# Optimization experiments

Hardware: AMD Instinct MI355X
Metric: run time of the kernel (lower is better)

Reference implementation:

```python
import jax, jax.numpy as jnp
import numpy as np
from jax import lax

NH = 8        # num_heads
NWIN = 7      # n_win
TOPK = 4


def setup_inputs() -> dict:
    key = jax.random.key(0)
    ks = jax.random.split(key, 7)
    B, C, H, W = 16, 256, 56, 56
    x = jax.random.normal(ks[0], (B, C, H, W), dtype=jnp.float32)
    s = 1.0 / np.sqrt(C)
    qkv_w = jax.random.normal(ks[1], (3 * C, C), dtype=jnp.float32) * s   # 1x1 conv
    qkv_b = jnp.zeros((3 * C,), dtype=jnp.float32)
    lepe_w = jax.random.normal(ks[2], (C, 1, 5, 5), dtype=jnp.float32) * 0.2  # depthwise 5x5
    lepe_b = jnp.zeros((C,), dtype=jnp.float32)
    out_w = jax.random.normal(ks[3], (C, C), dtype=jnp.float32) * s       # 1x1 conv
    out_b = jnp.zeros((C,), dtype=jnp.float32)
    return {"x": x, "qkv_w": qkv_w, "qkv_b": qkv_b, "lepe_w": lepe_w,
            "lepe_b": lepe_b, "out_w": out_w, "out_b": out_b}


def reference(x, qkv_w, qkv_b, lepe_w, lepe_b, out_w, out_b):
    B, C, H, W = x.shape
    rs0, rs1 = max(1, H // NWIN), max(1, W // NWIN)   # region size (H,W assumed divisible)
    rh, rw = H // rs0, W // rs1
    nreg, reg = rh * rw, rs0 * rs1
    hd = C // NH
    scale = C ** (-0.5)

    # qkv projection (1x1 conv == channel matmul)
    qkv = jnp.einsum('bchw,oc->bohw', x, qkv_w) + qkv_b[None, :, None, None]
    q, k, v = jnp.split(qkv, 3, axis=1)

    # region-level pooling (avg_pool over exact region blocks)
    def pool(t):
        return t.reshape(B, C, rh, rs0, rw, rs1).mean(axis=(3, 5))  # (B,C,rh,rw)
    q_r = pool(q).reshape(B, C, nreg).transpose(0, 2, 1)   # (B, nreg, C)
    k_r = pool(k).reshape(B, C, nreg)                      # (B, C, nreg)
    a_r = q_r @ k_r                                        # (B, nreg, nreg)
    _, idx = lax.top_k(a_r, TOPK)                          # (B, nreg, topk)

    # grid -> sequence: (B,C,H,W) -> (B,NH,nreg,reg,hd)
    def g2s(t):
        t = t.reshape(B, NH, hd, rh, rs0, rw, rs1)
        t = t.transpose(0, 1, 3, 5, 4, 6, 2)  # b,m,h,w,p,q,d
        return t.reshape(B, NH, nreg, reg, hd)

    qs, ks_, vs = g2s(q), g2s(k), g2s(v)

    # gather top-k kv regions per query region
    idx_h = jnp.broadcast_to(idx[:, None], (B, NH, nreg, TOPK))
    gidx = idx_h.reshape(B, NH, nreg * TOPK)[..., None, None]   # (B,NH,nreg*topk,1,1)
    kg = jnp.take_along_axis(ks_, gidx, axis=2).reshape(B, NH, nreg, TOPK * reg, hd)
    vg = jnp.take_along_axis(vs, gidx, axis=2).reshape(B, NH, nreg, TOPK * reg, hd)

    attn = jax.nn.softmax(jnp.einsum('bhnrd,bhnkd->bhnrk', qs * scale, kg), axis=-1)
    out = jnp.einsum('bhnrk,bhnkd->bhnrd', attn, vg)  # (B,NH,nreg,reg,hd)

    # sequence -> grid
    out = out.reshape(B, NH, rh, rw, rs0, rs1, hd)
    out = out.transpose(0, 1, 6, 2, 4, 3, 5).reshape(B, C, H, W)

    # LePE: depthwise 5x5 conv on v
    lepe = lax.conv_general_dilated(v, lepe_w, (1, 1), 'SAME',
                                    feature_group_count=C,
                                    dimension_numbers=('NCHW', 'OIHW', 'NCHW'))
    lepe = lepe + lepe_b[None, :, None, None]

    out = out + lepe
    out = jnp.einsum('bchw,oc->bohw', out, out_w) + out_b[None, :, None, None]
    return out
```

## Files before the change

### kernel.cpp

```cpp
#include <hip/hip_runtime.h>

typedef __attribute__((ext_vector_type(8))) short short8;
typedef __attribute__((ext_vector_type(4))) float f32x4;
typedef unsigned int uint;

constexpr int Bn    = 16;
constexpr int Cn    = 256;
constexpr int Hn    = 56;
constexpr int Wn    = 56;
constexpr int HWn   = Hn * Wn;
constexpr int NPn   = 3200;
constexpr int NHn   = 8;
constexpr int RWn   = 7;
constexpr int NREGn = 49;
constexpr int TOPKn = 4;
constexpr float QKSf = 0.0625f * 1.44269504088896f;

__device__ __forceinline__ float b2f(ushort u) { return __builtin_bit_cast(float, (uint)u << 16); }
__device__ __forceinline__ float b2fl(uint u) { return __builtin_bit_cast(float, u << 16); }
__device__ __forceinline__ float b2fh(uint u) { return __builtin_bit_cast(float, u & 0xffff0000u); }
__device__ __forceinline__ uint cvtpk(float lo, float hi) {
    uint r;
    asm("v_cvt_pk_bf16_f32 %0, %1, %2" : "=v"(r) : "v"(lo), "v"(hi));
    return r;
}

typedef __attribute__((address_space(3))) uint lds_u32_t;
typedef __attribute__((address_space(1))) const uint glb_u32_t;
__device__ __forceinline__ void gl_lds16(const ushort* g, ushort* l) {
    __builtin_amdgcn_global_load_lds((glb_u32_t*)g, (lds_u32_t*)l, 16, 0, 0);
}

__global__ __launch_bounds__(256)
void convert_w(const float* __restrict__ qw, const float* __restrict__ ow,
               ushort* __restrict__ wq, ushort* __restrict__ wo)
{
    const int e = (blockIdx.x * 256 + threadIdx.x) * 4;
    if (e < 196608) {
        const float4 v = *(const float4*)(qw + e);
        uint2 w; w.x = cvtpk(v.x, v.y); w.y = cvtpk(v.z, v.w);
        *(uint2*)(wq + e) = w;
    } else {
        const int e2 = e - 196608;
        const float4 v = *(const float4*)(ow + e2);
        uint2 w; w.x = cvtpk(v.x, v.y); w.y = cvtpk(v.z, v.w);
        *(uint2*)(wo + e2) = w;
    }
}

__global__ __launch_bounds__(256)
void convert_x(const float* __restrict__ x, ushort* __restrict__ xt,
               float* __restrict__ part)
{
    __shared__ float tile[64][65];
    const int p0 = blockIdx.x * 64, c0 = blockIdx.y * 64, b = blockIdx.z;
    const int tid = threadIdx.x;
    #pragma unroll
    for (int it = 0; it < 4; ++it) {
        const int slot = it * 256 + tid;
        const int c = slot >> 4, p4 = (slot & 15) << 2;
        const float4 v = *(const float4*)(x + ((size_t)b * Cn + c0 + c) * HWn + p0 + p4);
        tile[c][p4 + 0] = v.x; tile[c][p4 + 1] = v.y;
        tile[c][p4 + 2] = v.z; tile[c][p4 + 3] = v.w;
    }
    __syncthreads();
    #pragma unroll
    for (int it = 0; it < 4; ++it) {
        const int slot = it * 256 + tid;
        const int p = slot >> 4, c4 = (slot & 15) << 2;
        uint2 w;
        w.x = cvtpk(tile[c4 + 0][p], tile[c4 + 1][p]);
        w.y = cvtpk(tile[c4 + 2][p], tile[c4 + 3][p]);
        *(uint2*)(xt + ((size_t)b * NPn + p0 + p) * Cn + c0 + c4) = w;
    }
    {
        const int c = tid >> 2, q = tid & 3;
        float sA = 0.f, sB = 0.f;
        #pragma unroll
        for (int p = 0; p < 8; ++p) sA += tile[c][q * 16 + p];
        #pragma unroll
        for (int p = 0; p < 8; ++p) sB += tile[c][q * 16 + 8 + p];
        float* pp = part + ((((size_t)b * 4 + blockIdx.y) * 49 + blockIdx.x) * 64 + c) * 8 + q * 2;
        *(float2*)pp = make_float2(sA, sB);
    }
}

__global__ __launch_bounds__(256)
void reduce_pool(const float* __restrict__ part, float* __restrict__ xr)
{
    const int gid = blockIdx.x * 256 + threadIdx.x;
    const int r = gid % NREGn;
    const int t = gid / NREGn;
    const int c = t % Cn, b = t / Cn;
    const int ry = r / 7, rx = r % 7;
    const float* pb = part + ((((size_t)b * 4 + (c >> 6)) * 49 + 7 * ry) * 64 + (c & 63)) * 8;
    float s = 0.f;
    #pragma unroll
    for (int j = 0; j < 7; ++j) {
        const int s0 = (rx - j + 7) % 7;
        s += pb[j * 512 + s0];
        if (s0 == 0) s += pb[j * 512 + 7];
    }
    xr[gid] = s * (1.0f / 64.0f);
}

__global__ __launch_bounds__(256)
void qkr_gemm(const float* __restrict__ qw, const float* __restrict__ qb,
              const float* __restrict__ xr, float* __restrict__ qr,
              float* __restrict__ kr)
{
    const int gid = blockIdx.x * 256 + threadIdx.x;
    const int j = gid % NREGn;
    const int t = gid / NREGn;
    const int m = t & 511;
    const int b = t >> 9;
    const float* wr = qw + (size_t)m * Cn;
    const float* xb = xr + (size_t)b * Cn * NREGn + j;
    float s = 0.f;
    #pragma unroll 8
    for (int c = 0; c < Cn; ++c)
        s = fmaf(wr[c], xb[c * NREGn], s);
    s += qb[m];
    if (m < Cn) qr[((size_t)b * Cn + m) * NREGn + j] = s;
    else        kr[((size_t)b * Cn + (m - Cn)) * NREGn + j] = s;
}

__global__ __launch_bounds__(256)
void routing(const float* __restrict__ qr, const float* __restrict__ kr,
             int* __restrict__ idxo)
{
    const int ig = blockIdx.x, b = blockIdx.y;
    __shared__ float ksh[Cn][NREGn];
    __shared__ float qsh[Cn][7];
    __shared__ float ar[7][NREGn];
    const float* qb = qr + (size_t)b * Cn * NREGn;
    const float* kb = kr + (size_t)b * Cn * NREGn;
    for (int e = threadIdx.x; e < Cn * NREGn; e += 256)
        ksh[e / NREGn][e % NREGn] = kb[e];
    for (int e = threadIdx.x; e < Cn * 7; e += 256)
        qsh[e / 7][e % 7] = qb[(e / 7) * NREGn + ig * 7 + (e % 7)];
    __syncthreads();
    for (int e = threadIdx.x; e < 7 * NREGn; e += 256) {
        const int il = e / NREGn, j = e % NREGn;
        float s = 0.f;
        for (int c = 0; c < Cn; ++c)
            s = fmaf(qsh[c][il], ksh[c][j], s);
        ar[il][j] = s;
    }
    __syncthreads();
    if (threadIdx.x < 7) {
        const int il = threadIdx.x;
        float bv0 = -3.0e38f, bv1 = -3.0e38f, bv2 = -3.0e38f, bv3 = -3.0e38f;
        int bi0 = 0, bi1 = 0, bi2 = 0, bi3 = 0;
        for (int j = 0; j < NREGn; ++j) {
            const float v = ar[il][j];
            if (v > bv3) {
                if (v > bv0)      { bv3=bv2; bi3=bi2; bv2=bv1; bi2=bi1; bv1=bv0; bi1=bi0; bv0=v; bi0=j; }
                else if (v > bv1) { bv3=bv2; bi3=bi2; bv2=bv1; bi2=bi1; bv1=v; bi1=j; }
                else if (v > bv2) { bv3=bv2; bi3=bi2; bv2=v; bi2=j; }
                else              { bv3=v; bi3=j; }
            }
        }
        int* o = idxo + ((size_t)b * NREGn + ig * 7 + il) * TOPKn;
        o[0] = bi0; o[1] = bi1; o[2] = bi2; o[3] = bi3;
    }
}

template<int MODE>
__global__ __launch_bounds__(256)
void gemm_mfma(const ushort* __restrict__ Wb, const float* __restrict__ bias,
               const ushort* __restrict__ Bt,
               ushort* __restrict__ oq, ushort* __restrict__ ok,
               ushort* __restrict__ ovt, float* __restrict__ of)
{
    constexpr int K = Cn;
    int bb, bx, by;
    {
        const int flat = blockIdx.x;
        if (MODE == 0) {
            const int sw = (flat & 7) * 300 + (flat >> 3);
            bb = sw / 150; const int r2 = sw % 150; bx = r2 / 6; by = r2 % 6;
        } else {
            const int sw = (flat & 7) * 100 + (flat >> 3);
            bb = sw / 50;  const int r2 = sw % 50;  bx = r2 / 2; by = r2 % 2;
        }
    }
    const int n0 = bx * 128;
    const int m0 = by * 128;
    __shared__ ushort As[2][4096];
    __shared__ ushort Bs[2][4096];
    const int tid = threadIdx.x;
    const int wid = tid >> 6, lane = tid & 63;
    const int wm = wid >> 1, wn = wid & 1;
    const ushort* Bb = Bt + (size_t)bb * NPn * K;

    f32x4 acc[4][4];
    #pragma unroll
    for (int i = 0; i < 4; ++i)
        #pragma unroll
        for (int j = 0; j < 4; ++j)
            acc[i][j] = (f32x4){0.f, 0.f, 0.f, 0.f};

    const int cA = wid * 64 + lane;
    const int rowA = cA >> 2, koffA = (cA & 3) << 3;

    const ushort* wA0 = Wb + (size_t)(m0 + rowA) * K + koffA;
    const ushort* wA1 = Wb + (size_t)(m0 + rowA + 64) * K + koffA;
    const ushort* bB0 = Bb + (size_t)(n0 + rowA) * K + koffA;
    const ushort* bB1 = Bb + (size_t)(n0 + rowA + 64) * K + koffA;

#define STAGE(buf, k0)                                              \
    do {                                                            \
        gl_lds16(wA0 + (k0), &As[buf][wid * 512]);                  \
        gl_lds16(wA1 + (k0), &As[buf][2048 + wid * 512]);           \
        gl_lds16(bB0 + (k0), &Bs[buf][wid * 512]);                  \
        gl_lds16(bB1 + (k0), &Bs[buf][2048 + wid * 512]);           \
    } while (0)

    STAGE(0, 0);
    __syncthreads();
    int cur = 0;
    for (int k0 = 0; k0 < K; k0 += 32, cur ^= 1) {
        if (k0 + 32 < K) STAGE(cur ^ 1, k0 + 32);
        short8 a[4], b[4];
        #pragma unroll
        for (int i = 0; i < 4; ++i)
            a[i] = *(const short8*)(&As[cur][(wm * 64 + i * 16 + (lane & 15)) * 32 + ((lane >> 4) << 3)]);
        #pragma unroll
        for (int j = 0; j < 4; ++j)
            b[j] = *(const short8*)(&Bs[cur][(wn * 64 + j * 16 + (lane & 15)) * 32 + ((lane >> 4) << 3)]);
        #pragma unroll
        for (int i = 0; i < 4; ++i)
            #pragma unroll
            for (int j = 0; j < 4; ++j)
                acc[i][j] = __builtin_amdgcn_mfma_f32_16x16x32_bf16(a[i], b[j], acc[i][j], 0, 0, 0);
        __syncthreads();
    }
#undef STAGE

    if (MODE == 0) {
        #pragma unroll
        for (int i = 0; i < 4; ++i) {
            const int m_base = m0 + wm * 64 + i * 16;
            const int which = m_base >> 8;
            const int hh = (m_base >> 5) & 7;
            const int db = (m_base & 31) + ((lane >> 4) << 2);
            const float4 b4 = *(const float4*)(bias + m_base + ((lane >> 4) << 2));
            #pragma unroll
            for (int j = 0; j < 4; ++j) {
                const int n = n0 + wn * 64 + j * 16 + (lane & 15);
                if (n < HWn) {
                    const int py = n / 56, px = n % 56;
                    const int rr = (py >> 3) * 7 + (px >> 3);
                    const int ss = ((py & 7) << 3) + (px & 7);
                    if (which == 0) {
                        uint2 w;
                        w.x = cvtpk((acc[i][j][0] + b4.x) * QKSf, (acc[i][j][1] + b4.y) * QKSf);
                        w.y = cvtpk((acc[i][j][2] + b4.z) * QKSf, (acc[i][j][3] + b4.w) * QKSf);
                        *(uint2*)(oq + (((size_t)bb * NHn + hh) * HWn + rr * 64 + ss) * 32 + db) = w;
                    } else if (which == 1) {
                        uint2 w;
                        w.x = cvtpk(acc[i][j][0] + b4.x, acc[i][j][1] + b4.y);
                        w.y = cvtpk(acc[i][j][2] + b4.z, acc[i][j][3] + b4.w);
                        *(uint2*)(ok + (((size_t)bb * NHn + hh) * HWn + rr * 64 + ss) * 32 + db) = w;
                    } else {
                        const size_t vtb = ((size_t)(bb * NHn + hh) * 32 + db) * HWn + rr * 64 + ss;
                        const uint lo = cvtpk(acc[i][j][0] + b4.x, acc[i][j][1] + b4.y);
                        const uint hi = cvtpk(acc[i][j][2] + b4.z, acc[i][j][3] + b4.w);
                        ovt[vtb + 0 * HWn] = (ushort)lo;
                        ovt[vtb + 1 * HWn] = (ushort)(lo >> 16);
                        ovt[vtb + 2 * HWn] = (ushort)hi;
                        ovt[vtb + 3 * HWn] = (ushort)(hi >> 16);
                    }
                }
            }
        }
    } else {
        #pragma unroll
        for (int i = 0; i < 4; ++i) {
            const int mb = m0 + wm * 64 + i * 16 + ((lane >> 4) << 2);
            const float4 b4 = *(const float4*)(bias + mb);
            #pragma unroll
            for (int j = 0; j < 4; ++j) {
                const int n = n0 + wn * 64 + j * 16 + (lane & 15);
                if (n < HWn) {
                    const int rr = n >> 6, ss = n & 63;
                    const int py = (rr / 7) * 8 + (ss >> 3);
                    const int px = (rr % 7) * 8 + (ss & 7);
                    float* od = of + ((size_t)bb * Cn + mb) * HWn + py * 56 + px;
                    od[0 * HWn] = acc[i][j][0] + b4.x;
                    od[1 * HWn] = acc[i][j][1] + b4.y;
                    od[2 * HWn] = acc[i][j][2] + b4.z;
                    od[3 * HWn] = acc[i][j][3] + b4.w;
                }
            }
        }
    }
}

__global__ __launch_bounds__(256)
void lepe(const ushort* __restrict__ vt, const float* __restrict__ lw,
          const float* __restrict__ lb, ushort* __restrict__ lbuf)
{
    const int gid = blockIdx.x * 256 + threadIdx.x;
    const int plane = gid / 392;
    const int within = gid - plane * 392;
    const int row = within / 7;
    const int sx  = within - row * 7;
    const int px0 = sx * 8;
    const int c = plane & 255;
    const ushort* vp = vt + (size_t)plane * HWn;
    const float* wc = lw + c * 25;

    float wreg[25];
    #pragma unroll
    for (int i = 0; i < 25; ++i) wreg[i] = wc[i];

    float acc[8];
    const float bias = lb[c];
    #pragma unroll
    for (int j = 0; j < 8; ++j) acc[j] = bias;

    #pragma unroll
    for (int kh = 0; kh < 5; ++kh) {
        const int iy = row + kh - 2;
        if (iy < 0 || iy >= Hn) continue;
        const int ry = iy >> 3, il = iy & 7;
        const ushort* rp = vp + (ry * 7 + sx) * 64 + il * 8;
        const uint  a = *(const uint*)(rp - 64 + 6);
        const uint4 M = *(const uint4*)(rp);
        const uint  e = *(const uint*)(rp + 64);
        float w[12];
        w[0]  = (px0 >= 2)      ? b2fl(a)   : 0.f;
        w[1]  = (px0 >= 1)      ? b2fh(a)   : 0.f;
        w[2]  = b2fl(M.x); w[3]  = b2fh(M.x);
        w[4]  = b2fl(M.y); w[5]  = b2fh(M.y);
        w[6]  = b2fl(M.z); w[7]  = b2fh(M.z);
        w[8]  = b2fl(M.w); w[9]  = b2fh(M.w);
        w[10] = (px0 + 8 < Wn)  ? b2fl(e)   : 0.f;
        w[11] = (px0 + 9 < Wn)  ? b2fh(e)   : 0.f;
        #pragma unroll
        for (int kw = 0; kw < 5; ++kw) {
            const float ww = wreg[kh * 5 + kw];
            #pragma unroll
            for (int j = 0; j < 8; ++j)
                acc[j] = fmaf(w[j + kw], ww, acc[j]);
        }
    }
    ushort* op = lbuf + (size_t)plane * HWn + ((row >> 3) * 7 + sx) * 64 + (row & 7) * 8;
    uint2 wa, wb;
    wa.x = cvtpk(acc[0], acc[1]); wa.y = cvtpk(acc[2], acc[3]);
    wb.x = cvtpk(acc[4], acc[5]); wb.y = cvtpk(acc[6], acc[7]);
    *(uint2*)(op)     = wa;
    *(uint2*)(op + 4) = wb;
}

__global__ __launch_bounds__(256, 2)
void attention3(const ushort* __restrict__ qs, const ushort* __restrict__ ks,
                const ushort* __restrict__ vt, const int* __restrict__ idxp,
                const ushort* __restrict__ lep, ushort* __restrict__ yt)
{
    const int flat = blockIdx.x;
    const int sw = (flat & 7) * 196 + (flat >> 3);
    const int b = sw / 98;
    const int rem = sw % 98;
    const int r = rem % 49;
    const int wid = threadIdx.x >> 6, lane = threadIdx.x & 63;
    const int h = (rem / 49) * 4 + wid;
    const int col = lane & 15, g = lane >> 4;
    __shared__ ushort plds_all[4][4096];
    ushort* pw = plds_all[wid];

    const size_t hb = ((size_t)b * NHn + h) * HWn;
    const size_t vtb = (size_t)(b * NHn + h) * 32;

    short8 qf[4];
    #pragma unroll
    for (int qt = 0; qt < 4; ++qt)
        qf[qt] = *(const short8*)(qs + (hb + (size_t)r * 64 + qt * 16 + col) * 32 + g * 8);

    f32x4 o[4][2];
    #pragma unroll
    for (int qt = 0; qt < 4; ++qt) {
        o[qt][0] = (f32x4){0.f, 0.f, 0.f, 0.f};
        o[qt][1] = (f32x4){0.f, 0.f, 0.f, 0.f};
    }
    float mrow[4] = {-3.0e38f, -3.0e38f, -3.0e38f, -3.0e38f};
    float psum[4] = {0.f, 0.f, 0.f, 0.f};

    const int* ip = idxp + ((size_t)b * NREGn + r) * TOPKn;
    const int4 i4 = *(const int4*)ip;
    const int idxs[4] = {i4.x, i4.y, i4.z, i4.w};

    short8 kfA[4], vfA[4];
    {
        const int rr = idxs[0];
        #pragma unroll
        for (int kt = 0; kt < 4; ++kt)
            kfA[kt] = *(const short8*)(ks + (hb + (size_t)rr * 64 + kt * 16 + col) * 32 + g * 8);
        #pragma unroll
        for (int dt = 0; dt < 2; ++dt)
            #pragma unroll
            for (int kc = 0; kc < 2; ++kc)
                vfA[dt * 2 + kc] = *(const short8*)(vt + (vtb + dt * 16 + col) * HWn
                                                    + (size_t)rr * 64 + kc * 32 + g * 8);
    }

    #pragma unroll
    for (int t = 0; t < TOPKn; ++t) {
        short8 kfB[4], vfB[4];
        if (t < 3) {
            const int rr = idxs[t + 1];
            #pragma unroll
            for (int kt = 0; kt < 4; ++kt)
                kfB[kt] = *(const short8*)(ks + (hb + (size_t)rr * 64 + kt * 16 + col) * 32 + g * 8);
            #pragma unroll
            for (int dt = 0; dt < 2; ++dt)
                #pragma unroll
                for (int kc = 0; kc < 2; ++kc)
                    vfB[dt * 2 + kc] = *(const short8*)(vt + (vtb + dt * 16 + col) * HWn
                                                         + (size_t)rr * 64 + kc * 32 + g * 8);
        }

        #pragma unroll
        for (int qt = 0; qt < 4; ++qt) {
            f32x4 s[4];
            #pragma unroll
            for (int kt = 0; kt < 4; ++kt)
                s[kt] = __builtin_amdgcn_mfma_f32_16x16x32_bf16(
                    kfA[kt], qf[qt], (f32x4){0.f, 0.f, 0.f, 0.f}, 0, 0, 0);

            float mx = s[0][0];
            #pragma unroll
            for (int kt = 0; kt < 4; ++kt)
                #pragma unroll
                for (int e = 0; e < 4; ++e)
                    mx = fmaxf(mx, s[kt][e]);
            if (!__all(mx - mrow[qt] <= 8.f)) {
                float mr = mx;
                mr = fmaxf(mr, __shfl_xor(mr, 16));
                mr = fmaxf(mr, __shfl_xor(mr, 32));
                const float mnew = fmaxf(mrow[qt], mr);
                const float corr = exp2f(mrow[qt] - mnew);
                mrow[qt] = mnew;
                psum[qt] *= corr;
                #pragma unroll
                for (int reg = 0; reg < 4; ++reg) {
                    const float cr = __shfl(corr, g * 4 + reg);
                    o[qt][0][reg] *= cr;
                    o[qt][1][reg] *= cr;
                }
            }
            float ls = 0.f;
            #pragma unroll
            for (int kt = 0; kt < 4; ++kt)
                #pragma unroll
                for (int e = 0; e < 4; ++e) {
                    const float p = exp2f(s[kt][e] - mrow[qt]);
                    s[kt][e] = p; ls += p;
                }
            psum[qt] += ls;
            const int qrow = qt * 16 + col;
            const int swz = (qrow & 7) << 4;
            #pragma unroll
            for (int kt = 0; kt < 4; ++kt) {
                uint2 pk;
                pk.x = cvtpk(s[kt][0], s[kt][1]);
                pk.y = cvtpk(s[kt][2], s[kt][3]);
                const int byt = (qrow * 128 + kt * 32 + g * 8) ^ swz;
                *(uint2*)((char*)pw + byt) = pk;
            }
        }

        #pragma unroll
        for (int kc = 0; kc < 2; ++kc)
            #pragma unroll
            for (int qt = 0; qt < 4; ++qt) {
                const int qrow = qt * 16 + col;
                const int byt = (qrow * 128 + kc * 64 + g * 16) ^ ((qrow & 7) << 4);
                const short8 pf = *(const short8*)((const char*)pw + byt);
                o[qt][0] = __builtin_amdgcn_mfma_f32_16x16x32_bf16(pf, vfA[0 * 2 + kc], o[qt][0], 0, 0, 0);
                o[qt][1] = __builtin_amdgcn_mfma_f32_16x16x32_bf16(pf, vfA[1 * 2 + kc], o[qt][1], 0, 0, 0);
            }

        if (t < 3) {
            #pragma unroll
            for (int i = 0; i < 4; ++i) { kfA[i] = kfB[i]; vfA[i] = vfB[i]; }
        }
    }

    #pragma unroll
    for (int qt = 0; qt < 4; ++qt) {
        float ps = psum[qt];
        ps += __shfl_xor(ps, 16);
        ps += __shfl_xor(ps, 32);
        const float linv = 1.0f / ps;
        #pragma unroll
        for (int reg = 0; reg < 4; ++reg) {
            const float li = __shfl(linv, g * 4 + reg);
            const int row = qt * 16 + g * 4 + reg;
            const int swz = ((row >> 1) & 3) << 4;
            const uint pk = cvtpk(o[qt][0][reg] * li, o[qt][1][reg] * li);
            const int byt0 = (row * 64 + col * 2) ^ swz;
            const int byt1 = (row * 64 + (16 + col) * 2) ^ swz;
            *(ushort*)((char*)pw + byt0) = (ushort)pk;
            *(ushort*)((char*)pw + byt1) = (ushort)(pk >> 16);
        }
    }
    const ushort* lp = lep + ((size_t)b * Cn + h * 32) * HWn + (size_t)r * 64 + lane;
    ushort* yp = yt + ((size_t)b * NPn + (size_t)r * 64 + lane) * Cn + h * 32;
    const int swl = ((lane >> 1) & 3) << 4;
    #pragma unroll
    for (int c4 = 0; c4 < 8; ++c4) {
        const int byt = (lane * 64 + c4 * 8) ^ swl;
        const ushort4 ov = *(const ushort4*)((const char*)pw + byt);
        const float a0 = b2f(ov.x) + b2f(lp[(size_t)(c4 * 4 + 0) * HWn]);
        const float a1 = b2f(ov.y) + b2f(lp[(size_t)(c4 * 4 + 1) * HWn]);
        const float a2 = b2f(ov.z) + b2f(lp[(size_t)(c4 * 4 + 2) * HWn]);
        const float a3 = b2f(ov.w) + b2f(lp[(size_t)(c4 * 4 + 3) * HWn]);
        uint2 w4; w4.x = cvtpk(a0, a1); w4.y = cvtpk(a2, a3);
        *(uint2*)(yp + c4 * 4) = w4;
    }
}

extern "C" void kernel_launch(void* const* d_in, const int* in_sizes, int n_in,
                              void* d_out, int out_size, void* d_ws, size_t ws_size,
                              hipStream_t stream)
{
    const float* x      = (const float*)d_in[0];
    const float* qkv_w  = (const float*)d_in[1];
    const float* qkv_b  = (const float*)d_in[2];
    const float* lepe_w = (const float*)d_in[3];
    const float* lepe_b = (const float*)d_in[4];
    const float* out_w  = (const float*)d_in[5];
    const float* out_b  = (const float*)d_in[6];
    float* out = (float*)d_out;

    char* ws = (char*)d_ws;
    ushort* XT = (ushort*)(ws);
    ushort* YT = (ushort*)(ws + 26214400);
    ushort* QS = (ushort*)(ws + 52428800);
    ushort* KS = (ushort*)(ws + 78118912);
    ushort* VT = (ushort*)(ws + 103809024);
    ushort* LB = (ushort*)(ws + 129499136);
    ushort* WQ = (ushort*)(ws + 155189248);
    ushort* WO = (ushort*)(ws + 155582464);
    float*  XR = (float*)(ws + 155713536);
    float*  QR = (float*)(ws + 156516352);
    float*  KR = (float*)(ws + 157319168);
    int*   IDX = (int*)(ws + 158121984);
    float* PART = (float*)(ws + 158134528);

    convert_w<<<256, 256, 0, stream>>>(qkv_w, out_w, WQ, WO);
    convert_x<<<dim3(49, 4, 16), 256, 0, stream>>>(x, XT, PART);
    reduce_pool<<<784, 256, 0, stream>>>(PART, XR);
    qkr_gemm<<<1568, 256, 0, stream>>>(qkv_w, qkv_b, XR, QR, KR);
    routing<<<dim3(7, 16), 256, 0, stream>>>(QR, KR, IDX);
    gemm_mfma<0><<<2400, 256, 0, stream>>>(WQ, qkv_b, XT, QS, KS, VT, nullptr);
    lepe<<<6272, 256, 0, stream>>>(VT, lepe_w, lepe_b, LB);
    attention3<<<1568, 256, 0, stream>>>(QS, KS, VT, IDX, LB, YT);
    gemm_mfma<1><<<800, 256, 0, stream>>>(WO, out_b, YT, nullptr, nullptr, nullptr, out);
}
```

Before: 243.3 us.

## Fuse fp32-to-bf16 transpose of x into QKV GEMM B-tile loading

Removes the convert_x kernel and its bf16 transposed copy of x. The QKV GEMM now reads fp32 x directly with coalesced strided loads, converts to bf16 in registers and writes a padded (80-byte stride) LDS tile after the MFMA step. Region pooling is computed directly from x in a new pool_x kernel, replacing the partial-sum plus reduce pair. The attention running max is also initialised to 0 instead of a large negative value. The trade-off is that each of the six M-tiles per column block re-reads x in fp32 (twice the bytes of bf16) and conversion work moves into the GEMM's critical loop.

```diff
diff --git a/kernel.cpp b/kernel.cpp
--- a/kernel.cpp
+++ b/kernel.cpp
@@ -49,57 +49,20 @@
 }
 
 __global__ __launch_bounds__(256)
-void convert_x(const float* __restrict__ x, ushort* __restrict__ xt,
-               float* __restrict__ part)
-{
-    __shared__ float tile[64][65];
-    const int p0 = blockIdx.x * 64, c0 = blockIdx.y * 64, b = blockIdx.z;
-    const int tid = threadIdx.x;
-    #pragma unroll
-    for (int it = 0; it < 4; ++it) {
-        const int slot = it * 256 + tid;
-        const int c = slot >> 4, p4 = (slot & 15) << 2;
-        const float4 v = *(const float4*)(x + ((size_t)b * Cn + c0 + c) * HWn + p0 + p4);
-        tile[c][p4 + 0] = v.x; tile[c][p4 + 1] = v.y;
-        tile[c][p4 + 2] = v.z; tile[c][p4 + 3] = v.w;
-    }
-    __syncthreads();
-    #pragma unroll
-    for (int it = 0; it < 4; ++it) {
-        const int slot = it * 256 + tid;
-        const int p = slot >> 4, c4 = (slot & 15) << 2;
-        uint2 w;
-        w.x = cvtpk(tile[c4 + 0][p], tile[c4 + 1][p]);
-        w.y = cvtpk(tile[c4 + 2][p], tile[c4 + 3][p]);
-        *(uint2*)(xt + ((size_t)b * NPn + p0 + p) * Cn + c0 + c4) = w;
-    }
-    {
-        const int c = tid >> 2, q = tid & 3;
-        float sA = 0.f, sB = 0.f;
-        #pragma unroll
-        for (int p = 0; p < 8; ++p) sA += tile[c][q * 16 + p];
-        #pragma unroll
-        for (int p = 0; p < 8; ++p) sB += tile[c][q * 16 + 8 + p];
-        float* pp = part + ((((size_t)b * 4 + blockIdx.y) * 49 + blockIdx.x) * 64 + c) * 8 + q * 2;
-        *(float2*)pp = make_float2(sA, sB);
-    }
-}
-
-__global__ __launch_bounds__(256)
-void reduce_pool(const float* __restrict__ part, float* __restrict__ xr)
+void pool_x(const float* __restrict__ x, float* __restrict__ xr)
 {
     const int gid = blockIdx.x * 256 + threadIdx.x;
+    if (gid >= Bn * Cn * NREGn) return;
     const int r = gid % NREGn;
     const int t = gid / NREGn;
     const int c = t % Cn, b = t / Cn;
-    const int ry = r / 7, rx = r % 7;
-    const float* pb = part + ((((size_t)b * 4 + (c >> 6)) * 49 + 7 * ry) * 64 + (c & 63)) * 8;
+    const float* plane = x + ((size_t)b * Cn + c) * HWn + (r / RWn) * 8 * Wn + (r % RWn) * 8;
     float s = 0.f;
     #pragma unroll
-    for (int j = 0; j < 7; ++j) {
-        const int s0 = (rx - j + 7) % 7;
-        s += pb[j * 512 + s0];
-        if (s0 == 0) s += pb[j * 512 + 7];
+    for (int p = 0; p < 8; ++p) {
+        const float4 a  = *(const float4*)(plane + p * Wn);
+        const float4 b4 = *(const float4*)(plane + p * Wn + 4);
+        s += a.x + a.y + a.z + a.w + b4.x + b4.y + b4.z + b4.w;
     }
     xr[gid] = s * (1.0f / 64.0f);
 }
@@ -169,11 +132,12 @@
 template<int MODE>
 __global__ __launch_bounds__(256)
 void gemm_mfma(const ushort* __restrict__ Wb, const float* __restrict__ bias,
-               const ushort* __restrict__ Bt,
+               const ushort* __restrict__ Bt, const float* __restrict__ Xf,
                ushort* __restrict__ oq, ushort* __restrict__ ok,
                ushort* __restrict__ ovt, float* __restrict__ of)
 {
     constexpr int K = Cn;
+    constexpr int BSTR = (MODE == 0) ? 80 : 64;
     int bb, bx, by;
     {
         const int flat = blockIdx.x;
@@ -188,11 +152,10 @@
     const int n0 = bx * 128;
     const int m0 = by * 128;
     __shared__ ushort As[2][4096];
-    __shared__ ushort Bs[2][4096];
+    __shared__ ushort Bs[2][(MODE == 0) ? 5120 : 4096];
     const int tid = threadIdx.x;
     const int wid = tid >> 6, lane = tid & 63;
     const int wm = wid >> 1, wn = wid & 1;
-    const ushort* Bb = Bt + (size_t)bb * NPn * K;
 
     f32x4 acc[4][4];
     #pragma unroll
@@ -206,37 +169,84 @@
 
     const ushort* wA0 = Wb + (size_t)(m0 + rowA) * K + koffA;
     const ushort* wA1 = Wb + (size_t)(m0 + rowA + 64) * K + koffA;
-    const ushort* bB0 = Bb + (size_t)(n0 + rowA) * K + koffA;
-    const ushort* bB1 = Bb + (size_t)(n0 + rowA + 64) * K + koffA;
-
-#define STAGE(buf, k0)                                              \
+
+    const ushort* bB0 = nullptr; const ushort* bB1 = nullptr;
+    if constexpr (MODE == 1) {
+        const ushort* Bb = Bt + (size_t)bb * NPn * K;
+        bB0 = Bb + (size_t)(n0 + rowA) * K + koffA;
+        bB1 = Bb + (size_t)(n0 + rowA + 64) * K + koffA;
+    }
+    const float* xs = nullptr;
+    const int nl = tid & 127, kh = tid >> 7;
+    if constexpr (MODE == 0) {
+        const int nn = n0 + nl;
+        const int nc = nn < HWn ? nn : (HWn - 1);
+        xs = Xf + (size_t)bb * Cn * HWn + (size_t)kh * 16 * HWn + nc;
+    }
+    float fB[16];
+
+#define STAGEA(buf, k0)                                             \
     do {                                                            \
         gl_lds16(wA0 + (k0), &As[buf][wid * 512]);                  \
         gl_lds16(wA1 + (k0), &As[buf][2048 + wid * 512]);           \
+    } while (0)
+#define STAGEB1(buf, k0)                                            \
+    do {                                                            \
         gl_lds16(bB0 + (k0), &Bs[buf][wid * 512]);                  \
         gl_lds16(bB1 + (k0), &Bs[buf][2048 + wid * 512]);           \
     } while (0)
-
-    STAGE(0, 0);
+#define LOADB0(k0)                                                  \
+    do {                                                            \
+        _Pragma("unroll")                                           \
+        for (int j = 0; j < 16; ++j)                                \
+            fB[j] = xs[(size_t)((k0) + j) * HWn];                   \
+    } while (0)
+#define WRITEB0(buf)                                                \
+    do {                                                            \
+        uint4 wv0, wv1;                                             \
+        wv0.x = cvtpk(fB[0], fB[1]);   wv0.y = cvtpk(fB[2], fB[3]); \
+        wv0.z = cvtpk(fB[4], fB[5]);   wv0.w = cvtpk(fB[6], fB[7]); \
+        wv1.x = cvtpk(fB[8], fB[9]);   wv1.y = cvtpk(fB[10], fB[11]); \
+        wv1.z = cvtpk(fB[12], fB[13]); wv1.w = cvtpk(fB[14], fB[15]); \
+        char* bp = (char*)&Bs[buf][0] + nl * 80 + kh * 32;          \
+        *(uint4*)bp = wv0;                                          \
+        *(uint4*)(bp + 16) = wv1;                                   \
+    } while (0)
+
+    if constexpr (MODE == 0) LOADB0(0);
+    STAGEA(0, 0);
+    if constexpr (MODE == 1) STAGEB1(0, 0);
+    if constexpr (MODE == 0) WRITEB0(0);
     __syncthreads();
+
     int cur = 0;
     for (int k0 = 0; k0 < K; k0 += 32, cur ^= 1) {
-        if (k0 + 32 < K) STAGE(cur ^ 1, k0 + 32);
+        const bool more = (k0 + 32 < K);
+        if (more) {
+            if constexpr (MODE == 0) LOADB0(k0 + 32);
+            STAGEA(cur ^ 1, k0 + 32);
+            if constexpr (MODE == 1) STAGEB1(cur ^ 1, k0 + 32);
+        }
         short8 a[4], b[4];
         #pragma unroll
         for (int i = 0; i < 4; ++i)
             a[i] = *(const short8*)(&As[cur][(wm * 64 + i * 16 + (lane & 15)) * 32 + ((lane >> 4) << 3)]);
         #pragma unroll
         for (int j = 0; j < 4; ++j)
-            b[j] = *(const short8*)(&Bs[cur][(wn * 64 + j * 16 + (lane & 15)) * 32 + ((lane >> 4) << 3)]);
+            b[j] = *(const short8*)((const char*)&Bs[cur][0]
+                        + (wn * 64 + j * 16 + (lane & 15)) * BSTR + ((lane >> 4) << 4));
         #pragma unroll
         for (int i = 0; i < 4; ++i)
             #pragma unroll
             for (int j = 0; j < 4; ++j)
                 acc[i][j] = __builtin_amdgcn_mfma_f32_16x16x32_bf16(a[i], b[j], acc[i][j], 0, 0, 0);
+        if (more) { if constexpr (MODE == 0) WRITEB0(cur ^ 1); }
         __syncthreads();
     }
-#undef STAGE
+#undef STAGEA
+#undef STAGEB1
+#undef LOADB0
+#undef WRITEB0
 
     if (MODE == 0) {
         #pragma unroll
@@ -385,7 +395,7 @@
         o[qt][0] = (f32x4){0.f, 0.f, 0.f, 0.f};
         o[qt][1] = (f32x4){0.f, 0.f, 0.f, 0.f};
     }
-    float mrow[4] = {-3.0e38f, -3.0e38f, -3.0e38f, -3.0e38f};
+    float mrow[4] = {0.f, 0.f, 0.f, 0.f};
     float psum[4] = {0.f, 0.f, 0.f, 0.f};
 
     const int* ip = idxp + ((size_t)b * NREGn + r) * TOPKn;
@@ -537,7 +547,6 @@
     float* out = (float*)d_out;
 
     char* ws = (char*)d_ws;
-    ushort* XT = (ushort*)(ws);
     ushort* YT = (ushort*)(ws + 26214400);
     ushort* QS = (ushort*)(ws + 52428800);
     ushort* KS = (ushort*)(ws + 78118912);
@@ -549,15 +558,13 @@
     float*  QR = (float*)(ws + 156516352);
     float*  KR = (float*)(ws + 157319168);
     int*   IDX = (int*)(ws + 158121984);
-    float* PART = (float*)(ws + 158134528);
 
     convert_w<<<256, 256, 0, stream>>>(qkv_w, out_w, WQ, WO);
-    convert_x<<<dim3(49, 4, 16), 256, 0, stream>>>(x, XT, PART);
-    reduce_pool<<<784, 256, 0, stream>>>(PART, XR);
+    pool_x<<<(Bn * Cn * NREGn + 255) / 256, 256, 0, stream>>>(x, XR);
     qkr_gemm<<<1568, 256, 0, stream>>>(qkv_w, qkv_b, XR, QR, KR);
     routing<<<dim3(7, 16), 256, 0, stream>>>(QR, KR, IDX);
-    gemm_mfma<0><<<2400, 256, 0, stream>>>(WQ, qkv_b, XT, QS, KS, VT, nullptr);
+    gemm_mfma<0><<<2400, 256, 0, stream>>>(WQ, qkv_b, nullptr, x, QS, KS, VT, nullptr);
     lepe<<<6272, 256, 0, stream>>>(VT, lepe_w, lepe_b, LB);
     attention3<<<1568, 256, 0, stream>>>(QS, KS, VT, IDX, LB, YT);
-    gemm_mfma<1><<<800, 256, 0, stream>>>(WO, out_b, YT, nullptr, nullptr, nullptr, out);
-}
+    gemm_mfma<1><<<800, 256, 0, stream>>>(WO, out_b, YT, nullptr, nullptr, nullptr, nullptr, out);
+}
```

After: 233.7 us, median of 2. 1.04x faster.
